# Kernel optimization log

Measured on AMD Instinct MI355X. Metric: run time of the kernel, lower is better.

The kernel has to match this reference:

```python
import jax, jax.numpy as jnp
import numpy as np

VOCAB, EMB, HID, LAYERS, SEQ, BATCH = 128, 512, 1024, 2, 256, 64


def _lstm_layer(xs, h0, c0, Wih, Whh, b):
    # xs: [S, B, in], h0/c0: [B, H], Wih: [4H, in], Whh: [4H, H], b: [4H]
    def step(carry, x_t):
        h, c = carry
        gates = x_t @ Wih.T + h @ Whh.T + b  # [B, 4H]
        i, f, g, o = jnp.split(gates, 4, axis=-1)
        c = jax.nn.sigmoid(f) * c + jax.nn.sigmoid(i) * jnp.tanh(g)
        h = jax.nn.sigmoid(o) * jnp.tanh(c)
        return (h, c), h

    (h, c), ys = jax.lax.scan(step, (h0, c0), xs)
    return ys, h, c


def setup_inputs() -> dict:
    key = jax.random.key(0)
    ks = jax.random.split(key, 10)
    s = 0.05
    inp = {
        "x": jax.random.randint(ks[0], (SEQ, BATCH), 0, VOCAB),
        "h0": jnp.zeros((LAYERS, BATCH, HID), jnp.float32),
        "c0": jnp.zeros((LAYERS, BATCH, HID), jnp.float32),
        "emb": jax.random.normal(ks[1], (VOCAB, EMB), jnp.float32) * s,
        "Wih0": jax.random.normal(ks[2], (4 * HID, EMB), jnp.float32) * s,
        "Whh0": jax.random.normal(ks[3], (4 * HID, HID), jnp.float32) * s,
        "b0": jnp.zeros((4 * HID,), jnp.float32),
        "Wih1": jax.random.normal(ks[4], (4 * HID, HID), jnp.float32) * s,
        "Whh1": jax.random.normal(ks[5], (4 * HID, HID), jnp.float32) * s,
        "b1": jnp.zeros((4 * HID,), jnp.float32),
        "Wfc": jax.random.normal(ks[6], (VOCAB, HID), jnp.float32) * s,
        "bfc": jnp.zeros((VOCAB,), jnp.float32),
    }
    return inp


def reference(x, h0, c0, emb, Wih0, Whh0, b0, Wih1, Whh1, b1, Wfc, bfc):
    xs = emb[x]  # [S, B, EMB] embedding lookup
    ys0, h_0, c_0 = _lstm_layer(xs, h0[0], c0[0], Wih0, Whh0, b0)
    ys1, h_1, c_1 = _lstm_layer(ys0, h0[1], c0[1], Wih1, Whh1, b1)
    last = ys1[-1]  # [B, HID]
    logits = last @ Wfc.T + bfc  # [B, VOCAB]
    hidden = (jnp.stack([h_0, h_1]), jnp.stack([c_0, c_1]))
    return (logits, hidden)
```

## Files before the change

kernel.cpp:

```cpp
#include <hip/hip_runtime.h>
#include <hip/hip_bf16.h>

#define SEQ   256
#define BATCH 64
#define HID   1024
#define EMBD  512
#define VOCAB 128
#define G4    4096
#define HBS   (BATCH * HID)

typedef short bf16x8_t __attribute__((ext_vector_type(8)));
typedef float f32x4_t  __attribute__((ext_vector_type(4)));
using bf16 = __hip_bfloat16;

__device__ __forceinline__ float sigm(float v) { return 1.f / (1.f + expf(-v)); }

__device__ __forceinline__ void cstore4(void* p, unsigned d) {
    asm volatile("global_store_dword %0, %1, off sc0 sc1" :: "v"(p), "v"(d) : "memory");
}

__global__ void cast_f32_bf16(const float* __restrict__ src, bf16* __restrict__ dst, int n) {
    int i = blockIdx.x * blockDim.x + threadIdx.x;
    int stride = gridDim.x * blockDim.x;
    for (; i < n; i += stride) dst[i] = __float2bfloat16(src[i]);
}

__global__ void init_all(const float* __restrict__ h0,
                         bf16* __restrict__ r0, bf16* __restrict__ r1,
                         unsigned* __restrict__ flags) {
    int i = blockIdx.x * blockDim.x + threadIdx.x;
    if (i < 512) flags[i] = 0u;
    int stride = gridDim.x * blockDim.x;
    for (int k = i; k < HBS; k += stride) {
        r0[k] = __float2bfloat16(h0[k]);
        r1[k] = __float2bfloat16(h0[HBS + k]);
    }
}

__global__ __launch_bounds__(256) void emb_gemm(
    const bf16* __restrict__ emb_bf, const bf16* __restrict__ Wih0_bf,
    const float* __restrict__ b0, float* __restrict__ E) {
    __shared__ float pb[4 * 128 * 17];
    const int tid = threadIdx.x, l = tid & 63, w = tid >> 6;
    const int lm = l & 15, k8 = (l >> 4) << 3;
    const int colbase = blockIdx.x * 16;
    const int gcol = colbase + lm;
    const int kq = w * 128;

    f32x4_t acc[8];
    #pragma unroll
    for (int rt = 0; rt < 8; ++rt) acc[rt] = f32x4_t{0.f, 0.f, 0.f, 0.f};
    bf16x8_t bf[4];
    #pragma unroll
    for (int k = 0; k < 4; ++k)
        bf[k] = *reinterpret_cast<const bf16x8_t*>(Wih0_bf + gcol * EMBD + kq + k * 32 + k8);
    #pragma unroll
    for (int k = 0; k < 4; ++k)
        #pragma unroll
        for (int rt = 0; rt < 8; ++rt) {
            bf16x8_t a = *reinterpret_cast<const bf16x8_t*>(
                emb_bf + (rt * 16 + lm) * EMBD + kq + k * 32 + k8);
            acc[rt] = __builtin_amdgcn_mfma_f32_16x16x32_bf16(a, bf[k], acc[rt], 0, 0, 0);
        }
    const int r0 = (l >> 4) << 2;
    #pragma unroll
    for (int rt = 0; rt < 8; ++rt)
        #pragma unroll
        for (int r = 0; r < 4; ++r)
            pb[(w * 128 + rt * 16 + r0 + r) * 17 + lm] = acc[rt][r];
    __syncthreads();
    #pragma unroll
    for (int i = 0; i < 8; ++i) {
        int p = tid + i * 256;
        int m = p >> 4, cc = p & 15;
        float g = pb[(0 * 128 + m) * 17 + cc] + pb[(1 * 128 + m) * 17 + cc]
                + pb[(2 * 128 + m) * 17 + cc] + pb[(3 * 128 + m) * 17 + cc];
        E[m * G4 + colbase + cc] = g + b0[colbase + cc];
    }
}

__device__ __forceinline__ void stage_slice(const char* slotB, char* Aregion,
                                            int kByte, int l) {
    #pragma unroll
    for (int i = 0; i < 32; ++i) {
        const int ci  = i * 64 + l;
        const int row = ci >> 5, kb = ci & 31;
        const char* g = slotB + row * 2048 + kByte + ((kb ^ (row & 7)) << 4);
        __builtin_amdgcn_global_load_lds(
            (const __attribute__((address_space(1))) unsigned*)g,
            (__attribute__((address_space(3))) unsigned*)(Aregion + i * 1024),
            16, 0, 0);
    }
}

__device__ __forceinline__ void issue_w(bf16x8_t (&bw)[2][8], const bf16* W,
                                        int gcol0, int gcol1, int kg, int lk) {
    #pragma unroll
    for (int nt = 0; nt < 2; ++nt) {
        const bf16* wb = W + (size_t)(nt == 0 ? gcol0 : gcol1) * HID + kg * 256 + lk * 8;
        #pragma unroll
        for (int kc = 0; kc < 8; ++kc)
            bw[nt][kc] = *reinterpret_cast<const bf16x8_t*>(wb + kc * 32);
    }
}

__device__ __forceinline__ void gemm_compute(const char* Aregion,
                                             const bf16x8_t (&bw)[2][8],
                                             int lm, int lk, f32x4_t (&acc)[4][2]) {
    asm volatile("s_waitcnt vmcnt(0)" ::: "memory");
    __builtin_amdgcn_sched_barrier(0);
    #pragma unroll
    for (int kc = 0; kc < 8; ++kc) {
        bf16x8_t a[4];
        #pragma unroll
        for (int mt = 0; mt < 4; ++mt) {
            const int row = mt * 16 + lm;
            a[mt] = *reinterpret_cast<const bf16x8_t*>(
                Aregion + row * 512 + ((kc * 64 + lk * 16) ^ ((row & 7) << 4)));
        }
        #pragma unroll
        for (int mt = 0; mt < 4; ++mt) {
            acc[mt][0] = __builtin_amdgcn_mfma_f32_16x16x32_bf16(a[mt], bw[0][kc], acc[mt][0], 0, 0, 0);
            acc[mt][1] = __builtin_amdgcn_mfma_f32_16x16x32_bf16(a[mt], bw[1][kc], acc[mt][1], 0, 0, 0);
        }
    }
}

__device__ __forceinline__ void pollslice(const unsigned* fbase, int kg,
                                          unsigned target, int l) {
    const unsigned* fp = fbase + kg * 32 + (l & 31);
    bool ok = (__hip_atomic_load(fp, __ATOMIC_RELAXED,
                                 __HIP_MEMORY_SCOPE_AGENT) >= target);
    while (!__all((int)ok)) {
        __builtin_amdgcn_s_sleep(1);
        ok = (__hip_atomic_load(fp, __ATOMIC_RELAXED,
                                __HIP_MEMORY_SCOPE_AGENT) >= target);
    }
}

template<int GRP>
__device__ __forceinline__ void run_layer(
    const int* __restrict__ x,
    const bf16* __restrict__ Wx, const bf16* __restrict__ Wh,
    const float* __restrict__ E, const float* __restrict__ b1,
    const float* __restrict__ c0,
    bf16* __restrict__ rSelf, const bf16* __restrict__ rOther,
    unsigned* __restrict__ flags, float* __restrict__ out,
    char* __restrict__ Abuf, float* __restrict__ pbuf, int tid, int wg)
{
    const int gl = wg & 127;
    const int hb = gl * 8;
    const int l  = tid & 63, kg = tid >> 6;
    const int lm = l & 15, lk = l >> 4;
    char* Areg = Abuf + kg * 32768;
    const int kByte = kg * 512;

    const int gcol0 = (0 + (lm >> 3)) * HID + hb + (lm & 7);
    const int gcol1 = (2 + (lm >> 3)) * HID + hb + (lm & 7);

    const int am = tid >> 2, cp = tid & 3;
    const int cc0 = cp * 2, col0 = hb + cc0;
    float creg[2];
    creg[0] = c0[GRP * HBS + am * HID + col0];
    creg[1] = c0[GRP * HBS + am * HID + col0 + 1];

    const unsigned* fA = flags;
    const unsigned* fOwn = flags + GRP * 128;
    unsigned* fMine = (unsigned*)(fOwn + gl);

    const int s_begin = (GRP == 0) ? 0 : 1;
    const int s_end   = (GRP == 0) ? SEQ : SEQ + 1;

    for (int s = s_begin; s < s_end; ++s) {
        float ep[4][2];
        if (GRP == 0) {
            const int xv = x[s * BATCH + am];
            const float* Ep = E + (size_t)xv * G4 + col0;
            #pragma unroll
            for (int sec = 0; sec < 4; ++sec) {
                ep[sec][0] = Ep[sec * HID];
                ep[sec][1] = Ep[sec * HID + 1];
            }
        }

        f32x4_t acc[4][2];
        #pragma unroll
        for (int mt = 0; mt < 4; ++mt) {
            acc[mt][0] = f32x4_t{0.f, 0.f, 0.f, 0.f};
            acc[mt][1] = f32x4_t{0.f, 0.f, 0.f, 0.f};
        }

        if (GRP == 0) {
            bf16x8_t bw[2][8];
            issue_w(bw, Wh, gcol0, gcol1, kg, lk);
            pollslice(fOwn, kg, (unsigned)s, l);
            stage_slice((const char*)(rSelf + (size_t)s * HBS), Areg, kByte, l);
            gemm_compute(Areg, bw, lm, lk, acc);
        } else {
            bf16x8_t bw[2][8];
            issue_w(bw, Wx, gcol0, gcol1, kg, lk);
            pollslice(fA, kg, (unsigned)s, l);
            stage_slice((const char*)(rOther + (size_t)s * HBS), Areg, kByte, l);
            gemm_compute(Areg, bw, lm, lk, acc);
            asm volatile("s_waitcnt lgkmcnt(0)" ::: "memory");
            __builtin_amdgcn_sched_barrier(0);
            issue_w(bw, Wh, gcol0, gcol1, kg, lk);
            pollslice(fOwn, kg, (unsigned)(s - 1), l);
            stage_slice((const char*)(rSelf + (size_t)(s - 1) * HBS), Areg, kByte, l);
            gemm_compute(Areg, bw, lm, lk, acc);
        }

        if (kg < 2) {
            #pragma unroll
            for (int mt = 0; mt < 4; ++mt)
                #pragma unroll
                for (int nt = 0; nt < 2; ++nt)
                    #pragma unroll
                    for (int r = 0; r < 4; ++r)
                        pbuf[(kg * 64 + mt * 16 + lk * 4 + r) * 34 + nt * 16 + lm]
                            = acc[mt][nt][r];
        }
        __syncthreads();
        if (kg >= 2) {
            #pragma unroll
            for (int mt = 0; mt < 4; ++mt)
                #pragma unroll
                for (int nt = 0; nt < 2; ++nt)
                    #pragma unroll
                    for (int r = 0; r < 4; ++r) {
                        float* p = &pbuf[((kg - 2) * 64 + mt * 16 + lk * 4 + r) * 34
                                         + nt * 16 + lm];
                        *p += acc[mt][nt][r];
                    }
        }
        __syncthreads();

        float g[4][2];
        #pragma unroll
        for (int sec = 0; sec < 4; ++sec) {
            const float* p0 = &pbuf[(0 * 64 + am) * 34 + sec * 8 + cc0];
            const float* p1 = &pbuf[(1 * 64 + am) * 34 + sec * 8 + cc0];
            g[sec][0] = p0[0] + p1[0];
            g[sec][1] = p0[1] + p1[1];
        }
        if (GRP == 0) {
            #pragma unroll
            for (int sec = 0; sec < 4; ++sec) {
                g[sec][0] += ep[sec][0];
                g[sec][1] += ep[sec][1];
            }
        } else {
            #pragma unroll
            for (int sec = 0; sec < 4; ++sec) {
                g[sec][0] += b1[sec * HID + col0];
                g[sec][1] += b1[sec * HID + col0 + 1];
            }
        }

        float hn[2];
        #pragma unroll
        for (int j = 0; j < 2; ++j) {
            float si = sigm(g[0][j]);
            float sf = sigm(g[1][j]);
            float tg = tanhf(g[2][j]);
            float so = sigm(g[3][j]);
            float cn = sf * creg[j] + si * tg;
            hn[j] = so * tanhf(cn);
            creg[j] = cn;
        }
        unsigned short u0 = __builtin_bit_cast(unsigned short, __float2bfloat16(hn[0]));
        unsigned short u1 = __builtin_bit_cast(unsigned short, __float2bfloat16(hn[1]));
        const int wslot = (GRP == 0) ? s + 1 : s;
        cstore4(rSelf + (size_t)wslot * HBS + am * HID + col0,
                (unsigned)u0 | ((unsigned)u1 << 16));

        const bool last = (GRP == 0) ? (s == SEQ - 1) : (s == SEQ);
        if (last) {
            float* oh = out + BATCH * VOCAB + GRP * HBS;
            float* oc = out + BATCH * VOCAB + 2 * HBS + GRP * HBS;
            oh[am * HID + col0]     = hn[0];
            oh[am * HID + col0 + 1] = hn[1];
            oc[am * HID + col0]     = creg[0];
            oc[am * HID + col0 + 1] = creg[1];
        }

        asm volatile("s_waitcnt vmcnt(0)" ::: "memory");
        __syncthreads();
        if (tid == 0) cstore4(fMine, (unsigned)wslot);
    }
}

__global__ __launch_bounds__(256, 1) void lstm_persist(
    const int* __restrict__ x,
    const bf16* __restrict__ Whh0, const bf16* __restrict__ Wih1,
    const bf16* __restrict__ Whh1,
    const float* __restrict__ E, const float* __restrict__ b1,
    const float* __restrict__ c0,
    bf16* __restrict__ r0, bf16* __restrict__ r1,
    unsigned* __restrict__ flags, float* __restrict__ out)
{
    __shared__ char lds[131072 + 2 * 64 * 34 * 4];
    char*  Abuf = lds;
    float* pbuf = (float*)(lds + 131072);
    const int tid = threadIdx.x, wg = blockIdx.x;
    if (wg < 128)
        run_layer<0>(x, nullptr, Whh0, E, nullptr, c0, r0, nullptr, flags, out,
                     Abuf, pbuf, tid, wg);
    else
        run_layer<1>(x, Wih1, Whh1, E, b1, c0, r1, r0, flags, out,
                     Abuf, pbuf, tid, wg);
}

__global__ void logits_kernel(const float* __restrict__ h, const float* __restrict__ Wfc,
                              const float* __restrict__ bfc, float* __restrict__ out) {
    int t = blockIdx.x * blockDim.x + threadIdx.x;
    if (t >= BATCH * VOCAB) return;
    int m = t >> 7, v = t & 127;
    const float4* hp = reinterpret_cast<const float4*>(h + (size_t)m * HID);
    const float4* wp = reinterpret_cast<const float4*>(Wfc + (size_t)v * HID);
    float acc = 0.f;
    #pragma unroll 4
    for (int k = 0; k < HID / 4; ++k) {
        float4 a = hp[k], w = wp[k];
        acc += a.x * w.x + a.y * w.y + a.z * w.z + a.w * w.w;
    }
    out[t] = acc + bfc[v];
}

extern "C" void kernel_launch(void* const* d_in, const int* in_sizes, int n_in,
                              void* d_out, int out_size, void* d_ws, size_t ws_size,
                              hipStream_t stream) {
    const int*   x    = (const int*)d_in[0];
    const float* h0   = (const float*)d_in[1];
    const float* c0   = (const float*)d_in[2];
    const float* emb  = (const float*)d_in[3];
    const float* Wih0 = (const float*)d_in[4];
    const float* Whh0 = (const float*)d_in[5];
    const float* b0   = (const float*)d_in[6];
    const float* Wih1 = (const float*)d_in[7];
    const float* Whh1 = (const float*)d_in[8];
    const float* b1   = (const float*)d_in[9];
    const float* Wfc  = (const float*)d_in[10];
    const float* bfc  = (const float*)d_in[11];
    float* out = (float*)d_out;

    char* ws = (char*)d_ws;
    size_t off = 0;
    auto alloc = [&](size_t bytes) -> void* {
        void* p = ws + off;
        off += (bytes + 255) & ~(size_t)255;
        return p;
    };
    bf16*  Whh0_bf = (bf16*)alloc((size_t)G4 * HID * 2);
    bf16*  Wih1_bf = (bf16*)alloc((size_t)G4 * HID * 2);
    bf16*  Whh1_bf = (bf16*)alloc((size_t)G4 * HID * 2);
    float* E       = (float*)alloc((size_t)VOCAB * G4 * 4);
    bf16*  r0      = (bf16*)alloc((size_t)(SEQ + 1) * HBS * 2);
    bf16*  r1      = (bf16*)alloc((size_t)(SEQ + 1) * HBS * 2);
    unsigned* flags = (unsigned*)alloc(512 * 4);
    bf16* Wih0_bf  = (bf16*)alloc((size_t)G4 * EMBD * 2);
    bf16* emb_bf   = (bf16*)alloc((size_t)VOCAB * EMBD * 2);
    (void)ws_size; (void)in_sizes; (void)n_in; (void)out_size;

    cast_f32_bf16<<<64,  256, 0, stream>>>(emb,  emb_bf,  VOCAB * EMBD);
    cast_f32_bf16<<<512, 256, 0, stream>>>(Wih0, Wih0_bf, G4 * EMBD);
    cast_f32_bf16<<<512, 256, 0, stream>>>(Whh0, Whh0_bf, G4 * HID);
    cast_f32_bf16<<<512, 256, 0, stream>>>(Wih1, Wih1_bf, G4 * HID);
    cast_f32_bf16<<<512, 256, 0, stream>>>(Whh1, Whh1_bf, G4 * HID);
    init_all<<<64, 256, 0, stream>>>(h0, r0, r1, flags);
    emb_gemm<<<G4 / 16, 256, 0, stream>>>(emb_bf, Wih0_bf, b0, E);

    lstm_persist<<<256, 256, 0, stream>>>(x, Whh0_bf, Wih1_bf, Whh1_bf,
                                          E, b1, c0, r0, r1, flags, out);

    logits_kernel<<<(BATCH * VOCAB + 255) / 256, 256, 0, stream>>>(
        out + BATCH * VOCAB + HBS, Wfc, bfc, out);
}
```

Baseline: 2.233 ms.

## Compute layer-1 input projection for next step right after publishing current step

In the persistent two-layer LSTM kernel, layer-1 workgroups now run the Wih1·h0 partial GEMM for step s+1 immediately after signalling step s, instead of at the start of the next iteration. A prologue handles the first step. This takes the input-projection work off the critical path between the layer-1 recurrent dependency (own flag for s-1) and the gate update, so only the Whh GEMM waits on the recurrence. Accumulator registers now live across the loop boundary, which may raise register pressure, and the order of layer-0 polling changes.

Result: faster. 1.900 ms (-14.9%).

```diff
diff --git a/kernel.cpp b/kernel.cpp
--- a/kernel.cpp
+++ b/kernel.cpp
@@ -171,6 +171,26 @@
     const int s_begin = (GRP == 0) ? 0 : 1;
     const int s_end   = (GRP == 0) ? SEQ : SEQ + 1;
 
+    f32x4_t acc[4][2];
+    auto zacc = [&]() {
+        #pragma unroll
+        for (int mt = 0; mt < 4; ++mt) {
+            acc[mt][0] = f32x4_t{0.f, 0.f, 0.f, 0.f};
+            acc[mt][1] = f32x4_t{0.f, 0.f, 0.f, 0.f};
+        }
+    };
+
+    if (GRP == 1) {
+        zacc();
+        bf16x8_t bwx[2][8];
+        issue_w(bwx, Wx, gcol0, gcol1, kg, lk);
+        pollslice(fA, kg, 1u, l);
+        stage_slice((const char*)(rOther + (size_t)1 * HBS), Areg, kByte, l);
+        gemm_compute(Areg, bwx, lm, lk, acc);
+        asm volatile("s_waitcnt lgkmcnt(0)" ::: "memory");
+        __builtin_amdgcn_sched_barrier(0);
+    }
+
     for (int s = s_begin; s < s_end; ++s) {
         float ep[4][2];
         if (GRP == 0) {
@@ -181,32 +201,19 @@
                 ep[sec][0] = Ep[sec * HID];
                 ep[sec][1] = Ep[sec * HID + 1];
             }
-        }
-
-        f32x4_t acc[4][2];
-        #pragma unroll
-        for (int mt = 0; mt < 4; ++mt) {
-            acc[mt][0] = f32x4_t{0.f, 0.f, 0.f, 0.f};
-            acc[mt][1] = f32x4_t{0.f, 0.f, 0.f, 0.f};
-        }
-
-        if (GRP == 0) {
+            zacc();
+        }
+
+        {
             bf16x8_t bw[2][8];
             issue_w(bw, Wh, gcol0, gcol1, kg, lk);
-            pollslice(fOwn, kg, (unsigned)s, l);
-            stage_slice((const char*)(rSelf + (size_t)s * HBS), Areg, kByte, l);
-            gemm_compute(Areg, bw, lm, lk, acc);
-        } else {
-            bf16x8_t bw[2][8];
-            issue_w(bw, Wx, gcol0, gcol1, kg, lk);
-            pollslice(fA, kg, (unsigned)s, l);
-            stage_slice((const char*)(rOther + (size_t)s * HBS), Areg, kByte, l);
-            gemm_compute(Areg, bw, lm, lk, acc);
-            asm volatile("s_waitcnt lgkmcnt(0)" ::: "memory");
-            __builtin_amdgcn_sched_barrier(0);
-            issue_w(bw, Wh, gcol0, gcol1, kg, lk);
-            pollslice(fOwn, kg, (unsigned)(s - 1), l);
-            stage_slice((const char*)(rSelf + (size_t)(s - 1) * HBS), Areg, kByte, l);
+            if (GRP == 0) {
+                pollslice(fOwn, kg, (unsigned)s, l);
+                stage_slice((const char*)(rSelf + (size_t)s * HBS), Areg, kByte, l);
+            } else {
+                pollslice(fOwn, kg, (unsigned)(s - 1), l);
+                stage_slice((const char*)(rSelf + (size_t)(s - 1) * HBS), Areg, kByte, l);
+            }
             gemm_compute(Areg, bw, lm, lk, acc);
         }
 
@@ -287,6 +294,17 @@
         asm volatile("s_waitcnt vmcnt(0)" ::: "memory");
         __syncthreads();
         if (tid == 0) cstore4(fMine, (unsigned)wslot);
+
+        if (GRP == 1 && s + 1 < s_end) {
+            zacc();
+            bf16x8_t bwx[2][8];
+            issue_w(bwx, Wx, gcol0, gcol1, kg, lk);
+            pollslice(fA, kg, (unsigned)(s + 1), l);
+            stage_slice((const char*)(rOther + (size_t)(s + 1) * HBS), Areg, kByte, l);
+            gemm_compute(Areg, bwx, lm, lk, acc);
+            asm volatile("s_waitcnt lgkmcnt(0)" ::: "memory");
+            __builtin_amdgcn_sched_barrier(0);
+        }
     }
 }
 
```
